# Kernel tuning notes

Measured on AMD Instinct MI355X. Metric: run time of the kernel, lower is better.

The kernel has to match this reference:

```python
import jax, jax.numpy as jnp
import numpy as np

N, E, F, R, L, B = 50000, 800000, 64, 20, 2, 64
RC = 5.0
ZMAX = 100
LN2 = 0.6931471805599453

def ssp(x):
    # shifted softplus: softplus(x) - log(2)
    return jax.nn.softplus(x) - LN2

def setup_inputs() -> dict:
    key = jax.random.key(0)
    ks = jax.random.split(key, 32)
    w = lambda i, shape: jax.random.normal(ks[i], shape, dtype=jnp.float32) * 0.05
    inp = {
        'z': jax.random.randint(ks[0], (N,), 0, ZMAX + 1),
        'pos': jax.random.normal(ks[1], (N, 3), dtype=jnp.float32) * 3.0,
        'edge_index': jax.random.randint(ks[2], (2, E), 0, N),
        'batch_idx': jnp.sort(jax.random.randint(ks[3], (N,), 0, B)),
        'emb': jax.random.normal(ks[4], (ZMAX + 1, F), dtype=jnp.float32),
        'phi_W': w(5, (L, 3 * F, F)), 'phi_b': w(6, (L, 3 * F)),
        'filt_W1': w(7, (L, F, R)), 'filt_b1': w(8, (L, F)),
        'filt_W2': w(9, (L, 3 * F, F)), 'filt_b2': w(10, (L, 3 * F)),
        'U_W': w(11, (L, F, F)), 'V_W': w(12, (L, F, F)),
        'a_W1': w(13, (L, F, 2 * F)), 'a_b1': w(14, (L, F)),
        'a_W2': w(15, (L, 3 * F, F)), 'a_b2': w(16, (L, 3 * F)),
        'e_W1': w(17, (F // 2, F)), 'e_b1': w(18, (F // 2,)),
        'e_W2': w(19, (1, F // 2)), 'e_b2': w(20, (1,)),
        'dip_w': w(21, (F,)),
    }
    return inp

def reference(z, pos, edge_index, batch_idx, emb, phi_W, phi_b,
              filt_W1, filt_b1, filt_W2, filt_b2, U_W, V_W,
              a_W1, a_b1, a_W2, a_b2, e_W1, e_b1, e_W2, e_b2, dip_w):
    src, dst = edge_index[0], edge_index[1]
    s = emb[z]                               # (N, F)
    v = jnp.zeros((N, F, 3), dtype=s.dtype)  # (N, F, 3)

    # edge geometry
    r_vec = pos[dst] - pos[src]              # (E, 3)
    r_norm = jnp.linalg.norm(r_vec, axis=-1)
    r_hat = r_vec / jnp.maximum(r_norm, 1e-8)[:, None]
    # Gaussian RBF on [0, RC], widths = grid spacing
    mu = jnp.linspace(0.0, RC, R, dtype=s.dtype)
    width = mu[1] - mu[0]
    e_ij = jnp.exp(-((r_norm[:, None] - mu[None, :]) ** 2) / (2.0 * width * width))
    fc = 0.5 * (jnp.cos(jnp.pi * r_norm / RC) + 1.0) * (r_norm < RC)
    e_ij = e_ij * fc[:, None]                # (E, R)

    for l in range(L):
        # message block
        filt = ssp(e_ij @ filt_W1[l].T + filt_b1[l]) @ filt_W2[l].T + filt_b2[l]  # (E, 3F)
        W_s, W_v, W_r = jnp.split(filt, 3, axis=-1)
        phi = s[dst] @ phi_W[l].T + phi_b[l]                                       # (E, 3F)
        phi_s, phi_v, phi_r = jnp.split(phi, 3, axis=-1)
        m_s = W_s * phi_s                                                          # (E, F)
        m_v = W_v[:, :, None] * v[dst] + (W_r * phi_r)[:, :, None] * r_hat[:, None, :]  # (E, F, 3)
        s = s + jax.ops.segment_sum(m_s, src, num_segments=N)
        v = v + jax.ops.segment_sum(m_v, src, num_segments=N)
        # update block
        Uv = jnp.einsum('nfd,gf->ngd', v, U_W[l])
        Vv = jnp.einsum('nfd,gf->ngd', v, V_W[l])
        Vv_norm_sq = jnp.sum(Vv * Vv, axis=-1)                                     # (N, F)
        a = ssp(jnp.concatenate([s, Vv_norm_sq], axis=-1) @ a_W1[l].T + a_b1[l]) @ a_W2[l].T + a_b2[l]
        a_ss, a_sv, a_vv = jnp.split(a, 3, axis=-1)
        inner = jnp.sum(Uv * Vv, axis=-1)
        s = s + a_ss + a_sv * inner
        v = v + a_vv[:, :, None] * Uv

    # heads
    eps_i = (ssp(s @ e_W1.T + e_b1) @ e_W2.T + e_b2)[:, 0]  # (N,)
    energy = jax.ops.segment_sum(eps_i, batch_idx, num_segments=B)
    mu_i = jnp.sum(v * dip_w[None, :, None], axis=1)         # (N, 3)
    mu_mol = jax.ops.segment_sum(mu_i, batch_idx, num_segments=B)
    dipole = jnp.linalg.norm(mu_mol, axis=-1)
    charges = jnp.zeros((N,), dtype=s.dtype)
    return energy, dipole, charges
```

## Files before the change

### kernel.cpp

```cpp
#include <hip/hip_runtime.h>
#include <math.h>

static constexpr int N  = 50000;
static constexpr int E  = 800000;
static constexpr int F  = 64;
static constexpr int R  = 20;
static constexpr int NL = 2;
static constexpr int B  = 64;
static constexpr float RC   = 5.0f;
static constexpr float LN2F = 0.6931471805599453f;
static constexpr float WIDTH  = RC / (R - 1);
static constexpr float INV2W2 = 1.0f / (2.0f * WIDTH * WIDTH);
static constexpr float PI_F = 3.14159265358979323846f;

static constexpr int   NB     = 4096;
static constexpr float DR     = RC / NB;
static constexpr float INV_DR = NB / RC;
static constexpr int   TROWS  = NB + 2;
static constexpr int   TENT   = NB + 1;

static constexpr int NBLK_SCAN = (N + 255) / 256;

typedef __attribute__((ext_vector_type(8))) short bf16x8;
typedef __attribute__((ext_vector_type(4))) float f32x4;

__device__ __forceinline__ float ssp_f(float x) {
    return fmaxf(x, 0.0f) + log1pf(__expf(-fabsf(x))) - LN2F;
}

__device__ __forceinline__ short f2bf(float x) {
    unsigned u = __builtin_bit_cast(unsigned, x);
    unsigned r = (u + 0x7fffu + ((u >> 16) & 1u)) >> 16;
    return (short)r;
}
__device__ __forceinline__ float bf_lo(unsigned u) {
    return __builtin_bit_cast(float, u << 16);
}
__device__ __forceinline__ float bf_hi(unsigned u) {
    return __builtin_bit_cast(float, u & 0xffff0000u);
}

__global__ void k_hist(const int* __restrict__ ei, int* __restrict__ cnt) {
    int e = blockIdx.x * blockDim.x + threadIdx.x;
    if (e < E) atomicAdd(&cnt[ei[e]], 1);
}

__global__ void k_scan_a(const int* __restrict__ cnt, int* __restrict__ bsum) {
    __shared__ int part[256];
    const int t = threadIdx.x;
    const int idx = blockIdx.x * 256 + t;
    int v = (idx < N) ? cnt[idx] : 0;
    part[t] = v;
    __syncthreads();
    for (int d = 1; d < 256; d <<= 1) {
        int x = (t >= d) ? part[t - d] : 0;
        __syncthreads();
        part[t] += x;
        __syncthreads();
    }
    if (t == 255) bsum[blockIdx.x] = part[255];
}

__global__ void k_scan_b(const int* __restrict__ bsum, int* __restrict__ bpre,
                         int* __restrict__ offN) {
    __shared__ int part[256];
    const int t = threadIdx.x;
    int v = (t < NBLK_SCAN) ? bsum[t] : 0;
    part[t] = v;
    __syncthreads();
    for (int d = 1; d < 256; d <<= 1) {
        int x = (t >= d) ? part[t - d] : 0;
        __syncthreads();
        part[t] += x;
        __syncthreads();
    }
    if (t < NBLK_SCAN) bpre[t] = part[t] - v;
    if (t == NBLK_SCAN - 1) *offN = part[t];
}

__global__ void k_scan_c(const int* __restrict__ cnt, const int* __restrict__ bpre,
                         int* __restrict__ off, int* __restrict__ cur) {
    __shared__ int part[256];
    const int t = threadIdx.x;
    const int idx = blockIdx.x * 256 + t;
    int v = (idx < N) ? cnt[idx] : 0;
    part[t] = v;
    __syncthreads();
    for (int d = 1; d < 256; d <<= 1) {
        int x = (t >= d) ? part[t - d] : 0;
        __syncthreads();
        part[t] += x;
        __syncthreads();
    }
    if (idx < N) {
        int e = bpre[blockIdx.x] + part[t] - v;
        off[idx] = e;
        cur[idx] = e;
    }
}

__global__ void k_scatter(const int* __restrict__ ei, int* __restrict__ cur,
                          const float* __restrict__ pos, uint4* __restrict__ edata) {
    int e = blockIdx.x * blockDim.x + threadIdx.x;
    if (e >= E) return;
    int src = ei[e], dst = ei[E + e];
    int p = atomicAdd(&cur[src], 1);
    float qx = pos[dst * 3 + 0] - pos[src * 3 + 0];
    float qy = pos[dst * 3 + 1] - pos[src * 3 + 1];
    float qz = pos[dst * 3 + 2] - pos[src * 3 + 2];
    float rn = sqrtf(qx * qx + qy * qy + qz * qz);
    float invn = 1.0f / fmaxf(rn, 1e-8f);
    float t = rn * INV_DR;
    int i = (int)t;
    float fr = t - (float)i;
    if (i >= NB) { i = NB; fr = 0.0f; }
    uint4 rec;
    rec.x = (unsigned)dst;
    rec.y = (unsigned)i | ((unsigned)(unsigned short)f2bf(fr) << 16);
    rec.z = (unsigned)(unsigned short)f2bf(qx * invn)
          | ((unsigned)(unsigned short)f2bf(qy * invn) << 16);
    rec.w = (unsigned)(unsigned short)f2bf(qz * invn);
    edata[p] = rec;
}

__global__ void k_table(const float* __restrict__ fW1, const float* __restrict__ fb1,
                        const float* __restrict__ fW2, const float* __restrict__ fb2,
                        unsigned short* __restrict__ Tp) {
    const int l   = blockIdx.x / TROWS;
    const int row = blockIdx.x % TROWS;
    const int lane = threadIdx.x;
    const float r = fminf((float)row, (float)NB) * DR;
    const float fc = (r < RC) ? 0.5f * (__cosf(PI_F * r * (1.0f / RC)) + 1.0f) : 0.0f;

    __shared__ float sh[F];
    float acc = fb1[l * F + lane];
    const float* w1 = fW1 + (size_t)l * F * R + (size_t)lane * R;
    #pragma unroll
    for (int rr = 0; rr < R; rr++) {
        float dmu = r - rr * WIDTH;
        float er = __expf(-dmu * dmu * INV2W2) * fc;
        acc = fmaf(er, w1[rr], acc);
    }
    sh[lane] = ssp_f(acc);
    __syncthreads();
    unsigned short* TpL = Tp + (size_t)l * TENT * 512;
    #pragma unroll
    for (int p = 0; p < 3; p++) {
        int c = p * 64 + lane;
        float a = fb2[l * 192 + c];
        const float* w2 = fW2 + ((size_t)l * 192 + c) * 64;
        #pragma unroll 8
        for (int k = 0; k < F; k++) a = fmaf(sh[k], w2[k], a);
        unsigned short bf = (unsigned short)f2bf(a);
        if (row <= NB) TpL[(size_t)row * 512 + lane * 8 + p * 2 + 0] = bf;
        if (row >= 1)  TpL[(size_t)(row - 1) * 512 + lane * 8 + p * 2 + 1] = bf;
    }
    if (row <= NB) {
        TpL[(size_t)row * 512 + lane * 8 + 6] = 0;
        TpL[(size_t)row * 512 + lane * 8 + 7] = 0;
    }
}

__launch_bounds__(256)
__global__ void k_pack0(float* __restrict__ s, const int* __restrict__ z,
                        const float* __restrict__ emb,
                        const float* __restrict__ PW, const float* __restrict__ Pb,
                        unsigned* __restrict__ ndA) {
    __shared__ float sbuf[4][F];
    const int lane = threadIdx.x & 63;
    const int wid  = threadIdx.x >> 6;
    const int gwave = blockIdx.x * 4 + wid;
    const int nwaves = gridDim.x * 4;

    float wsr[F], wrr[F];
    {
        const float* rs = PW + (size_t)lane * 64;
        const float* rr = PW + (size_t)(128 + lane) * 64;
        #pragma unroll
        for (int k = 0; k < F; k += 4) {
            float4 a = *(const float4*)(rs + k);
            wsr[k] = a.x; wsr[k+1] = a.y; wsr[k+2] = a.z; wsr[k+3] = a.w;
            float4 b = *(const float4*)(rr + k);
            wrr[k] = b.x; wrr[k+1] = b.y; wrr[k+2] = b.z; wrr[k+3] = b.w;
        }
    }
    const float bs = Pb[lane], br = Pb[128 + lane];

    for (int n = gwave; n < N; n += nwaves) {
        float sv = emb[(size_t)z[n] * F + lane];
        s[(size_t)n * F + lane] = sv;
        sbuf[wid][lane] = sv;
        float as = bs, ar = br;
        #pragma unroll
        for (int k = 0; k < F; k += 4) {
            float4 s4 = *(const float4*)&sbuf[wid][k];
            as = fmaf(s4.x, wsr[k],   as); as = fmaf(s4.y, wsr[k+1], as);
            as = fmaf(s4.z, wsr[k+2], as); as = fmaf(s4.w, wsr[k+3], as);
            ar = fmaf(s4.x, wrr[k],   ar); ar = fmaf(s4.y, wrr[k+1], ar);
            ar = fmaf(s4.z, wrr[k+2], ar); ar = fmaf(s4.w, wrr[k+3], ar);
        }
        ndA[(size_t)n * 64 + lane] = (unsigned)(unsigned short)f2bf(as)
                                   | ((unsigned)(unsigned short)f2bf(ar) << 16);
    }
}

template<bool ACCUMV>
__device__ __forceinline__ void edge_step(const uint4 ed,
                                          const unsigned short* __restrict__ TpL,
                                          const unsigned* __restrict__ ndA,
                                          const uint2* __restrict__ ndV, int lane,
                                          float& ms, float& mv0, float& mv1, float& mv2) {
    const int   i  = (int)(ed.y & 0xffffu);
    const float fr = bf_hi(ed.y);
    const uint4 t  = *(const uint4*)(TpL + (size_t)i * 512 + lane * 8);
    const unsigned a = ndA[(size_t)ed.x * 64 + lane];
    const float Ws = fmaf(fr, bf_hi(t.x) - bf_lo(t.x), bf_lo(t.x));
    const float Wr = fmaf(fr, bf_hi(t.z) - bf_lo(t.z), bf_lo(t.z));
    ms = fmaf(Ws, bf_lo(a), ms);
    const float c = Wr * bf_hi(a);
    const float rhx = bf_lo(ed.z), rhy = bf_hi(ed.z), rhz = bf_lo(ed.w);
    if (ACCUMV) {
        const float Wv = fmaf(fr, bf_hi(t.y) - bf_lo(t.y), bf_lo(t.y));
        const uint2 w = ndV[(size_t)ed.x * 64 + lane];
        mv0 = fmaf(Wv, bf_lo(w.x), fmaf(c, rhx, mv0));
        mv1 = fmaf(Wv, bf_hi(w.x), fmaf(c, rhy, mv1));
        mv2 = fmaf(Wv, bf_lo(w.y), fmaf(c, rhz, mv2));
    } else {
        mv0 = fmaf(c, rhx, mv0);
        mv1 = fmaf(c, rhy, mv1);
        mv2 = fmaf(c, rhz, mv2);
    }
}

template<bool ACCUMV>
__launch_bounds__(256)
__global__ void k_gather(const uint4* __restrict__ edata, const int* __restrict__ off,
                         const unsigned short* __restrict__ TpL,
                         const unsigned* __restrict__ ndA, const uint2* __restrict__ ndV,
                         float* __restrict__ s, float* __restrict__ v) {
    const int lane = threadIdx.x & 63;
    const int wid  = threadIdx.x >> 6;
    const int n = blockIdx.x * 4 + wid;
    if (n >= N) return;
    const int base = off[n], end = off[n + 1];
    float msA = 0.f, a0 = 0.f, a1 = 0.f, a2 = 0.f;
    float msB = 0.f, b0 = 0.f, b1 = 0.f, b2 = 0.f;

    int k = base;
    for (; k + 1 < end; k += 2) {
        const uint4 e0 = edata[k];
        const uint4 e1 = edata[k + 1];
        edge_step<ACCUMV>(e0, TpL, ndA, ndV, lane, msA, a0, a1, a2);
        edge_step<ACCUMV>(e1, TpL, ndA, ndV, lane, msB, b0, b1, b2);
    }
    if (k < end) {
        const uint4 e0 = edata[k];
        edge_step<ACCUMV>(e0, TpL, ndA, ndV, lane, msA, a0, a1, a2);
    }
    const float ms = msA + msB;
    const float mv0 = a0 + b0, mv1 = a1 + b1, mv2 = a2 + b2;

    s[(size_t)n * F + lane] += ms;
    float* vo = v + (size_t)n * 3 * F + lane;
    if (ACCUMV) {
        vo[0]     += mv0;
        vo[F]     += mv1;
        vo[2 * F] += mv2;
    } else {
        vo[0] = mv0; vo[F] = mv1; vo[2 * F] = mv2;
    }
}

__device__ __forceinline__ bf16x8 load_wfrag(const float* __restrict__ Wp, int ldk,
                                             int nrow, int k0) {
    const float* p = Wp + (size_t)nrow * ldk + k0;
    float4 a = *(const float4*)p;
    float4 b = *(const float4*)(p + 4);
    bf16x8 r;
    r[0] = f2bf(a.x); r[1] = f2bf(a.y); r[2] = f2bf(a.z); r[3] = f2bf(a.w);
    r[4] = f2bf(b.x); r[5] = f2bf(b.y); r[6] = f2bf(b.z); r[7] = f2bf(b.w);
    return r;
}

template<bool DO_PACK>
__launch_bounds__(256)
__global__ void k_update_mfma(float* __restrict__ s, float* __restrict__ v,
                              const float* __restrict__ U_W, const float* __restrict__ V_W,
                              const float* __restrict__ aW1, const float* __restrict__ ab1,
                              const float* __restrict__ aW2, const float* __restrict__ ab2,
                              const float* __restrict__ PW, const float* __restrict__ Pb,
                              unsigned* __restrict__ ndA, uint2* __restrict__ ndV) {
    __shared__ short vlds[96 * 72];
    __shared__ short xlds[32 * 136];
    __shared__ short hlds[32 * 72];

    const int tid = threadIdx.x;
    const int l   = tid & 63;
    const int w   = tid >> 6;
    const int lo  = l & 15;
    const int hi  = l >> 4;

    bf16x8 ufr[2], vfr[2], w1fr[4], w2fr[3][2];
    #pragma unroll
    for (int kk = 0; kk < 2; kk++) {
        ufr[kk] = load_wfrag(U_W, 64, w * 16 + lo, kk * 32 + hi * 8);
        vfr[kk] = load_wfrag(V_W, 64, w * 16 + lo, kk * 32 + hi * 8);
    }
    #pragma unroll
    for (int kk = 0; kk < 4; kk++)
        w1fr[kk] = load_wfrag(aW1, 128, w * 16 + lo, kk * 32 + hi * 8);
    #pragma unroll
    for (int p = 0; p < 3; p++)
        #pragma unroll
        for (int kk = 0; kk < 2; kk++)
            w2fr[p][kk] = load_wfrag(aW2, 64, p * 64 + w * 16 + lo, kk * 32 + hi * 8);

    bf16x8 pws[2], pwr[2];
    float pbs = 0.f, pbr = 0.f;
    if (DO_PACK) {
        #pragma unroll
        for (int kk = 0; kk < 2; kk++) {
            pws[kk] = load_wfrag(PW, 64, w * 16 + lo, kk * 32 + hi * 8);
            pwr[kk] = load_wfrag(PW, 64, 128 + w * 16 + lo, kk * 32 + hi * 8);
        }
        pbs = Pb[w * 16 + lo];
        pbr = Pb[128 + w * 16 + lo];
    }

    const float ab1c  = ab1[w * 16 + lo];
    const float ab2c0 = ab2[w * 16 + lo];
    const float ab2c1 = ab2[64 + w * 16 + lo];
    const float ab2c2 = ab2[128 + w * 16 + lo];
    const int g = w * 16 + lo;

    for (int half = 0; half < 2; half++) {
        const int n0 = blockIdx.x * 64 + half * 32;
        if (half) __syncthreads();

        for (int u = tid; u < 96 * 8; u += 256) {
            int row = u >> 3, oct = u & 7;
            int d = row >> 5, nn = row & 31;
            int n = min(n0 + nn, N - 1);
            const float* src = v + ((size_t)n * 3 + d) * 64 + oct * 8;
            float4 a = *(const float4*)src;
            float4 b = *(const float4*)(src + 4);
            bf16x8 t;
            t[0] = f2bf(a.x); t[1] = f2bf(a.y); t[2] = f2bf(a.z); t[3] = f2bf(a.w);
            t[4] = f2bf(b.x); t[5] = f2bf(b.y); t[6] = f2bf(b.z); t[7] = f2bf(b.w);
            *(bf16x8*)&vlds[row * 72 + oct * 8] = t;
        }
        for (int u = tid; u < 32 * 8; u += 256) {
            int nn = u >> 3, oct = u & 7;
            int n = min(n0 + nn, N - 1);
            const float* src = s + (size_t)n * 64 + oct * 8;
            float4 a = *(const float4*)src;
            float4 b = *(const float4*)(src + 4);
            bf16x8 t;
            t[0] = f2bf(a.x); t[1] = f2bf(a.y); t[2] = f2bf(a.z); t[3] = f2bf(a.w);
            t[4] = f2bf(b.x); t[5] = f2bf(b.y); t[6] = f2bf(b.z); t[7] = f2bf(b.w);
            *(bf16x8*)&xlds[nn * 136 + oct * 8] = t;
        }
        __syncthreads();

        f32x4 cu[6], cv[6];
        #pragma unroll
        for (int mt = 0; mt < 6; mt++) { cu[mt] = (f32x4)0.0f; cv[mt] = (f32x4)0.0f; }
        #pragma unroll
        for (int kk = 0; kk < 2; kk++) {
            #pragma unroll
            for (int mt = 0; mt < 6; mt++) {
                bf16x8 af = *(const bf16x8*)&vlds[(mt * 16 + lo) * 72 + kk * 32 + hi * 8];
                cu[mt] = __builtin_amdgcn_mfma_f32_16x16x32_bf16(af, ufr[kk], cu[mt], 0, 0, 0);
                cv[mt] = __builtin_amdgcn_mfma_f32_16x16x32_bf16(af, vfr[kk], cv[mt], 0, 0, 0);
            }
        }

        f32x4 inn[2];
        #pragma unroll
        for (int nt = 0; nt < 2; nt++) {
            #pragma unroll
            for (int r = 0; r < 4; r++) {
                float vs = 0.f, ii = 0.f;
                #pragma unroll
                for (int d = 0; d < 3; d++) {
                    float a = cu[d * 2 + nt][r], b = cv[d * 2 + nt][r];
                    vs = fmaf(b, b, vs);
                    ii = fmaf(a, b, ii);
                }
                inn[nt][r] = ii;
                int nl = nt * 16 + hi * 4 + r;
                xlds[nl * 136 + 64 + w * 16 + lo] = f2bf(vs);
            }
        }
        __syncthreads();

        f32x4 c2[2];
        c2[0] = (f32x4)0.0f; c2[1] = (f32x4)0.0f;
        #pragma unroll
        for (int kk = 0; kk < 4; kk++) {
            #pragma unroll
            for (int mt = 0; mt < 2; mt++) {
                bf16x8 af = *(const bf16x8*)&xlds[(mt * 16 + lo) * 136 + kk * 32 + hi * 8];
                c2[mt] = __builtin_amdgcn_mfma_f32_16x16x32_bf16(af, w1fr[kk], c2[mt], 0, 0, 0);
            }
        }
        #pragma unroll
        for (int mt = 0; mt < 2; mt++)
            #pragma unroll
            for (int r = 0; r < 4; r++) {
                float hv = ssp_f(c2[mt][r] + ab1c);
                hlds[(mt * 16 + hi * 4 + r) * 72 + w * 16 + lo] = f2bf(hv);
            }
        __syncthreads();

        f32x4 c3[2][3];
        #pragma unroll
        for (int mt = 0; mt < 2; mt++)
            #pragma unroll
            for (int p = 0; p < 3; p++) c3[mt][p] = (f32x4)0.0f;
        #pragma unroll
        for (int kk = 0; kk < 2; kk++) {
            #pragma unroll
            for (int mt = 0; mt < 2; mt++) {
                bf16x8 af = *(const bf16x8*)&hlds[(mt * 16 + lo) * 72 + kk * 32 + hi * 8];
                #pragma unroll
                for (int p = 0; p < 3; p++)
                    c3[mt][p] = __builtin_amdgcn_mfma_f32_16x16x32_bf16(af, w2fr[p][kk], c3[mt][p], 0, 0, 0);
            }
        }

        float snew[2][4];
        #pragma unroll
        for (int mt = 0; mt < 2; mt++) {
            #pragma unroll
            for (int r = 0; r < 4; r++) {
                int n = n0 + mt * 16 + hi * 4 + r;
                if (n >= N) { snew[mt][r] = 0.f; continue; }
                float a_ss = c3[mt][0][r] + ab2c0;
                float a_sv = c3[mt][1][r] + ab2c1;
                float a_vv = c3[mt][2][r] + ab2c2;
                size_t si = (size_t)n * 64 + g;
                float sn = s[si] + a_ss + a_sv * inn[mt][r];
                s[si] = sn;
                snew[mt][r] = sn;
                float vn[3];
                #pragma unroll
                for (int d = 0; d < 3; d++) {
                    size_t vi = ((size_t)n * 3 + d) * 64 + g;
                    vn[d] = v[vi] + a_vv * cu[d * 2 + mt][r];
                    v[vi] = vn[d];
                }
                if (DO_PACK) {
                    uint2 pv;
                    pv.x = (unsigned)(unsigned short)f2bf(vn[0])
                         | ((unsigned)(unsigned short)f2bf(vn[1]) << 16);
                    pv.y = (unsigned)(unsigned short)f2bf(vn[2]);
                    ndV[(size_t)n * 64 + g] = pv;
                }
            }
        }

        if (DO_PACK) {
            __syncthreads();
            #pragma unroll
            for (int mt = 0; mt < 2; mt++)
                #pragma unroll
                for (int r = 0; r < 4; r++)
                    hlds[(mt * 16 + hi * 4 + r) * 72 + g] = f2bf(snew[mt][r]);
            __syncthreads();

            f32x4 cs[2], cr[2];
            cs[0] = (f32x4)0.0f; cs[1] = (f32x4)0.0f;
            cr[0] = (f32x4)0.0f; cr[1] = (f32x4)0.0f;
            #pragma unroll
            for (int kk = 0; kk < 2; kk++) {
                #pragma unroll
                for (int mt = 0; mt < 2; mt++) {
                    bf16x8 af = *(const bf16x8*)&hlds[(mt * 16 + lo) * 72 + kk * 32 + hi * 8];
                    cs[mt] = __builtin_amdgcn_mfma_f32_16x16x32_bf16(af, pws[kk], cs[mt], 0, 0, 0);
                    cr[mt] = __builtin_amdgcn_mfma_f32_16x16x32_bf16(af, pwr[kk], cr[mt], 0, 0, 0);
                }
            }
            #pragma unroll
            for (int mt = 0; mt < 2; mt++) {
                #pragma unroll
                for (int r = 0; r < 4; r++) {
                    int n = n0 + mt * 16 + hi * 4 + r;
                    if (n >= N) continue;
                    ndA[(size_t)n * 64 + g] =
                          (unsigned)(unsigned short)f2bf(cs[mt][r] + pbs)
                        | ((unsigned)(unsigned short)f2bf(cr[mt][r] + pbr) << 16);
                }
            }
        }
    }
}

__global__ void k_heads(const float* __restrict__ s, const float* __restrict__ v,
                        const int* __restrict__ batch_idx,
                        const float* __restrict__ eW1, const float* __restrict__ eb1,
                        const float* __restrict__ eW2, const float* __restrict__ eb2,
                        const float* __restrict__ dip_w,
                        float* __restrict__ eacc, float* __restrict__ macc) {
    __shared__ float se[B];
    __shared__ float sm[3][B];
    if (threadIdx.x < B) se[threadIdx.x] = 0.0f;
    if (threadIdx.x < 3 * B) sm[threadIdx.x >> 6][threadIdx.x & 63] = 0.0f;
    __syncthreads();
    int n = blockIdx.x * blockDim.x + threadIdx.x;
    if (n < N) {
        int b = batch_idx[n];
        float sr[F];
        #pragma unroll
        for (int f = 0; f < F; f += 4) {
            float4 t = *(const float4*)&s[(size_t)n * F + f];
            sr[f] = t.x; sr[f+1] = t.y; sr[f+2] = t.z; sr[f+3] = t.w;
        }
        float eps = eb2[0];
        for (int jj = 0; jj < F / 2; jj++) {
            float acc = eb1[jj];
            #pragma unroll
            for (int f = 0; f < F; f++)
                acc = fmaf(sr[f], eW1[jj * F + f], acc);
            eps = fmaf(eW2[jj], ssp_f(acc), eps);
        }
        atomicAdd(&se[b], eps);
        #pragma unroll
        for (int d = 0; d < 3; d++) {
            float m = 0.0f;
            #pragma unroll 8
            for (int f = 0; f < F; f++)
                m = fmaf(v[((size_t)n * 3 + d) * F + f], dip_w[f], m);
            atomicAdd(&sm[d][b], m);
        }
    }
    __syncthreads();
    if (threadIdx.x < B) atomicAdd(&eacc[threadIdx.x], se[threadIdx.x]);
    if (threadIdx.x >= B && threadIdx.x < 4 * B) {
        int d = (threadIdx.x >> 6) - 1, b = threadIdx.x & 63;
        atomicAdd(&macc[d * B + b], sm[d][b]);
    }
}

__global__ void k_final(const float* __restrict__ eacc, const float* __restrict__ macc,
                        float* __restrict__ out) {
    int b = threadIdx.x;
    if (b < B) {
        out[b] = eacc[b];
        float mx = macc[b], my = macc[B + b], mz = macc[2 * B + b];
        out[B + b] = sqrtf(mx * mx + my * my + mz * mz);
    }
}

extern "C" void kernel_launch(void* const* d_in, const int* in_sizes, int n_in,
                              void* d_out, int out_size, void* d_ws, size_t ws_size,
                              hipStream_t stream) {
    const int*   z     = (const int*)d_in[0];
    const float* pos   = (const float*)d_in[1];
    const int*   ei    = (const int*)d_in[2];
    const int*   bidx  = (const int*)d_in[3];
    const float* emb   = (const float*)d_in[4];
    const float* phi_W = (const float*)d_in[5];
    const float* phi_b = (const float*)d_in[6];
    const float* fW1   = (const float*)d_in[7];
    const float* fb1   = (const float*)d_in[8];
    const float* fW2   = (const float*)d_in[9];
    const float* fb2   = (const float*)d_in[10];
    const float* U_W   = (const float*)d_in[11];
    const float* V_W   = (const float*)d_in[12];
    const float* aW1   = (const float*)d_in[13];
    const float* ab1   = (const float*)d_in[14];
    const float* aW2   = (const float*)d_in[15];
    const float* ab2   = (const float*)d_in[16];
    const float* eW1   = (const float*)d_in[17];
    const float* eb1   = (const float*)d_in[18];
    const float* eW2   = (const float*)d_in[19];
    const float* eb2   = (const float*)d_in[20];
    const float* dip_w = (const float*)d_in[21];
    float* out = (float*)d_out;

    float* ws = (float*)d_ws;
    float* s    = ws;
    float* v    = s + (size_t)N * F;
    unsigned* ndA = (unsigned*)(v + (size_t)N * F * 3);
    uint2* ndV  = (uint2*)(ndA + (size_t)N * 64);
    unsigned short* Tp = (unsigned short*)(ndV + (size_t)N * 64);
    float* eacc = (float*)(Tp + (size_t)NL * TENT * 512);
    float* macc = eacc + B;
    int*   cnt  = (int*)(macc + 3 * B);
    int*   off  = cnt  + N;
    int*   cur  = off  + N + 1;
    int*   bsum = cur  + N;
    int*   bpre = bsum + 256;
    uint4* edata = (uint4*)(((uintptr_t)(bpre + 256) + 15) & ~(uintptr_t)15);

    hipMemsetAsync(cnt,  0, sizeof(int) * N, stream);
    hipMemsetAsync(eacc, 0, sizeof(float) * 4 * B, stream);
    hipMemsetAsync(out + 2 * B, 0, sizeof(float) * (size_t)N, stream);

    k_hist<<<(E + 255) / 256, 256, 0, stream>>>(ei, cnt);
    k_scan_a<<<NBLK_SCAN, 256, 0, stream>>>(cnt, bsum);
    k_scan_b<<<1, 256, 0, stream>>>(bsum, bpre, off + N);
    k_scan_c<<<NBLK_SCAN, 256, 0, stream>>>(cnt, bpre, off, cur);
    k_scatter<<<(E + 255) / 256, 256, 0, stream>>>(ei, cur, pos, edata);
    k_table<<<NL * TROWS, 64, 0, stream>>>(fW1, fb1, fW2, fb2, Tp);

    const int gblocks = (N + 3) / 4;
    const int ublocks = (N + 63) / 64;
    k_pack0<<<512, 256, 0, stream>>>(s, z, emb, phi_W, phi_b, ndA);
    k_gather<false><<<gblocks, 256, 0, stream>>>(edata, off, Tp, ndA, ndV, s, v);
    k_update_mfma<true><<<ublocks, 256, 0, stream>>>(s, v,
        U_W, V_W, aW1, ab1, aW2, ab2,
        phi_W + (size_t)192 * 64, phi_b + 192, ndA, ndV);
    k_gather<true><<<gblocks, 256, 0, stream>>>(edata, off,
        Tp + (size_t)TENT * 512, ndA, ndV, s, v);
    k_update_mfma<false><<<ublocks, 256, 0, stream>>>(s, v,
        U_W + 4096, V_W + 4096, aW1 + 8192, ab1 + F, aW2 + 12288, ab2 + 192,
        nullptr, nullptr, nullptr, nullptr);

    k_heads<<<(N + 255) / 256, 256, 0, stream>>>(s, v, bidx, eW1, eb1, eW2, eb2,
                                                 dip_w, eacc, macc);
    k_final<<<1, 64, 0, stream>>>(eacc, macc, out);
}
```

Baseline: 562.1 us.

## Split each node's edge gather across four waves with LDS reduction

The gather kernel now assigns one node per 256-thread block instead of one node per wave. The node's edges are interleaved across the four waves, and the per-wave partial sums are combined through shared memory before a single write. Each wave also prefetches its next edge record while processing the current one. This aims to shorten per-node serial latency chains and expose more memory-level parallelism. In exchange it adds a __syncthreads and an LDS reduction per node, quadruples the block count, and leaves waves idle on nodes with few edges (about 16 on average).

Measured after the change: 555.4 us. Within noise of the previous version (-1.2%).

```diff
diff --git a/kernel.cpp b/kernel.cpp
--- a/kernel.cpp
+++ b/kernel.cpp
@@ -233,41 +233,51 @@
 }
 
 template<bool ACCUMV>
-__launch_bounds__(256)
+__launch_bounds__(256, 1)
 __global__ void k_gather(const uint4* __restrict__ edata, const int* __restrict__ off,
                          const unsigned short* __restrict__ TpL,
                          const unsigned* __restrict__ ndA, const uint2* __restrict__ ndV,
                          float* __restrict__ s, float* __restrict__ v) {
+    __shared__ float red[4][4][64];
     const int lane = threadIdx.x & 63;
-    const int wid  = threadIdx.x >> 6;
-    const int n = blockIdx.x * 4 + wid;
-    if (n >= N) return;
+    const int wv   = threadIdx.x >> 6;
+    const int n = blockIdx.x;
     const int base = off[n], end = off[n + 1];
-    float msA = 0.f, a0 = 0.f, a1 = 0.f, a2 = 0.f;
-    float msB = 0.f, b0 = 0.f, b1 = 0.f, b2 = 0.f;
-
-    int k = base;
-    for (; k + 1 < end; k += 2) {
-        const uint4 e0 = edata[k];
-        const uint4 e1 = edata[k + 1];
-        edge_step<ACCUMV>(e0, TpL, ndA, ndV, lane, msA, a0, a1, a2);
-        edge_step<ACCUMV>(e1, TpL, ndA, ndV, lane, msB, b0, b1, b2);
-    }
+
+    float ms = 0.f, mv0 = 0.f, mv1 = 0.f, mv2 = 0.f;
+    int k = base + wv;
     if (k < end) {
-        const uint4 e0 = edata[k];
-        edge_step<ACCUMV>(e0, TpL, ndA, ndV, lane, msA, a0, a1, a2);
-    }
-    const float ms = msA + msB;
-    const float mv0 = a0 + b0, mv1 = a1 + b1, mv2 = a2 + b2;
-
-    s[(size_t)n * F + lane] += ms;
-    float* vo = v + (size_t)n * 3 * F + lane;
-    if (ACCUMV) {
-        vo[0]     += mv0;
-        vo[F]     += mv1;
-        vo[2 * F] += mv2;
-    } else {
-        vo[0] = mv0; vo[F] = mv1; vo[2 * F] = mv2;
+        uint4 ed = edata[k];
+        for (;;) {
+            const int kn = k + 4;
+            const bool more = kn < end;
+            uint4 edn;
+            if (more) edn = edata[kn];
+            edge_step<ACCUMV>(ed, TpL, ndA, ndV, lane, ms, mv0, mv1, mv2);
+            if (!more) break;
+            ed = edn;
+            k = kn;
+        }
+    }
+    red[wv][0][lane] = ms;
+    red[wv][1][lane] = mv0;
+    red[wv][2][lane] = mv1;
+    red[wv][3][lane] = mv2;
+    __syncthreads();
+    if (wv == 0) {
+        ms  = red[0][0][lane] + red[1][0][lane] + red[2][0][lane] + red[3][0][lane];
+        mv0 = red[0][1][lane] + red[1][1][lane] + red[2][1][lane] + red[3][1][lane];
+        mv1 = red[0][2][lane] + red[1][2][lane] + red[2][2][lane] + red[3][2][lane];
+        mv2 = red[0][3][lane] + red[1][3][lane] + red[2][3][lane] + red[3][3][lane];
+        s[(size_t)n * F + lane] += ms;
+        float* vo = v + (size_t)n * 3 * F + lane;
+        if (ACCUMV) {
+            vo[0]     += mv0;
+            vo[F]     += mv1;
+            vo[2 * F] += mv2;
+        } else {
+            vo[0] = mv0; vo[F] = mv1; vo[2 * F] = mv2;
+        }
     }
 }
 
@@ -605,14 +615,13 @@
     k_scatter<<<(E + 255) / 256, 256, 0, stream>>>(ei, cur, pos, edata);
     k_table<<<NL * TROWS, 64, 0, stream>>>(fW1, fb1, fW2, fb2, Tp);
 
-    const int gblocks = (N + 3) / 4;
     const int ublocks = (N + 63) / 64;
     k_pack0<<<512, 256, 0, stream>>>(s, z, emb, phi_W, phi_b, ndA);
-    k_gather<false><<<gblocks, 256, 0, stream>>>(edata, off, Tp, ndA, ndV, s, v);
+    k_gather<false><<<N, 256, 0, stream>>>(edata, off, Tp, ndA, ndV, s, v);
     k_update_mfma<true><<<ublocks, 256, 0, stream>>>(s, v,
         U_W, V_W, aW1, ab1, aW2, ab2,
         phi_W + (size_t)192 * 64, phi_b + 192, ndA, ndV);
-    k_gather<true><<<gblocks, 256, 0, stream>>>(edata, off,
+    k_gather<true><<<N, 256, 0, stream>>>(edata, off,
         Tp + (size_t)TENT * 512, ndA, ndV, s, v);
     k_update_mfma<false><<<ublocks, 256, 0, stream>>>(s, v,
         U_W + 4096, V_W + 4096, aW1 + 8192, ab1 + F, aW2 + 12288, ab2 + 192,
```
